# Kernel tuning notes

Hardware: AMD Instinct MI355X
Metric: run time of the kernel (lower is better)

## Reference

```python
import jax, jax.numpy as jnp
import numpy as np

NU = 0.01 / np.pi  # viscosity buffer from the torch module


def _mlp(x, W_in, b_in, W_hid, b_hid, W_out, b_out):
    # x: [N, 2] -> u: [N, 1]; tanh MLP with stacked hidden layers scanned.
    h = jnp.tanh(x @ W_in + b_in)

    def step(h, wb):
        W, b = wb
        return jnp.tanh(h @ W + b), None

    h, _ = jax.lax.scan(step, h, (W_hid, b_hid))
    return h @ W_out + b_out


def setup_inputs() -> dict:
    key = jax.random.key(0)
    ks = jax.random.split(key, 10)
    N_f, N0, Nb, H, L = 131072, 4096, 2048, 128, 7
    s_in = 1.0 / np.sqrt(2.0)
    s_h = 1.0 / np.sqrt(H)
    return {
        "x_f": jax.random.normal(ks[0], (N_f, 2), jnp.float32),
        "x0_cat": jax.random.normal(ks[1], (N0, 2), jnp.float32),
        "xb_left_cat": jax.random.normal(ks[2], (Nb, 2), jnp.float32),
        "xb_right_cat": jax.random.normal(ks[3], (Nb, 2), jnp.float32),
        "W_in": jax.random.normal(ks[4], (2, H), jnp.float32) * s_in,
        "b_in": jax.random.normal(ks[5], (H,), jnp.float32) * 0.01,
        "W_hid": jax.random.normal(ks[6], (L, H, H), jnp.float32) * s_h,
        "b_hid": jax.random.normal(ks[7], (L, H), jnp.float32) * 0.01,
        "W_out": jax.random.normal(ks[8], (H, 1), jnp.float32) * s_h,
        "b_out": jax.random.normal(ks[9], (1,), jnp.float32) * 0.01,
    }


def reference(x_f, x0_cat, xb_left_cat, xb_right_cat,
              W_in, b_in, W_hid, b_hid, W_out, b_out):
    u = lambda x: _mlp(x, W_in, b_in, W_hid, b_hid, W_out, b_out)

    u_0_pred = u(x0_cat)
    u_b_left_pred = u(xb_left_cat)
    u_b_right_pred = u(xb_right_cat)

    u_f_pred = u(x_f)  # [N_f, 1]

    # Each row of u depends only on the matching row of x, so grad of the sum
    # yields per-example gradients (equivalent to torch.autograd.grad with
    # grad_outputs=ones).
    usum = lambda x: u(x).sum()
    g = jax.grad(usum)(x_f)            # [N_f, 2]
    u_x = g[:, 0:1]
    u_t = g[:, 1:2]

    # Second derivative: grad of sum(u_x) w.r.t. x, take the x-component.
    uxx_full = jax.grad(lambda x: jax.grad(usum)(x)[:, 0].sum())(x_f)
    u_xx = uxx_full[:, 0:1]

    pde_residual = u_t + u_f_pred * u_x - NU * u_xx
    return jnp.concatenate((u_0_pred, u_b_left_pred, u_b_right_pred,
                            pde_residual), axis=0)
```

## Files before the change

### kernel.cpp

```cpp
#include <hip/hip_runtime.h>
#include <math.h>

#define NU_F 0.0031830988618379067f

typedef _Float16 f16x8 __attribute__((ext_vector_type(8)));
typedef float    f32x4 __attribute__((ext_vector_type(4)));

__device__ __forceinline__ float fast_tanh(float z) {
    float e = __builtin_amdgcn_exp2f(2.885390082f * z);
    float r = __builtin_amdgcn_rcpf(e + 1.0f);
    return fmaf(-2.0f, r, 1.0f);
}

__device__ __forceinline__ unsigned pkf16(float a, float b) {
    auto v = __builtin_amdgcn_cvt_pkrtz(a, b);
    return __builtin_bit_cast(unsigned, v);
}

__global__ void prep_wfrag(const float* __restrict__ Whid, _Float16* __restrict__ wcf)
{
    const int t    = blockIdx.x * 256 + threadIdx.x;
    const int lane = t & 63;
    const int fid  = t >> 6;
    const int ks = fid & 3;
    const int nt = (fid >> 2) & 7;
    const int l  = fid >> 5;
    const int q  = lane >> 4;
    const int nn = lane & 15;
    const int c  = ((nt >> 2) << 6) + nn * 4 + (nt & 3);
    const int k0 = ks * 32 + q * 8;
    const float* src = Whid + l * 16384 + k0 * 128 + c;
    f16x8 v;
    #pragma unroll
    for (int jj = 0; jj < 8; ++jj)
        v[jj] = (_Float16)src[jj * 128];
    *(f16x8*)(wcf + (size_t)t * 8) = v;
}

#define HR 68
#define MFMA(A, B, C) __builtin_amdgcn_mfma_f32_16x16x32_f16((A), (B), (C), 0, 0, 0)

__global__ __launch_bounds__(128, 3)
void pinn_fused(const float* __restrict__ xf,
                const float* __restrict__ x0,  const float* __restrict__ xbl,
                const float* __restrict__ xbr,
                const float* __restrict__ Win,  const float* __restrict__ bin,
                const float* __restrict__ bhid,
                const float* __restrict__ Wout, const float* __restrict__ bout,
                const _Float16* __restrict__ wcf,
                float* __restrict__ out)
{
    __shared__ unsigned Hh[64 * HR];
    __shared__ float xpt[128];
    __shared__ float pbuf[128];
    __shared__ float dots[64];

    const int tid  = threadIdx.x;
    const int lane = tid & 63;
    const int wv   = tid >> 6;
    const int lm   = lane & 15;
    const int lq   = lane >> 4;
    const int blk  = blockIdx.x;
    const bool isv = (blk >= 8192);

    if (!isv) {
        if (tid < 32) xpt[tid] = xf[blk * 32 + tid];
    } else {
        const int vb = blk - 8192;
        const float* src = (vb < 64) ? (x0 + vb * 128)
                         : (vb < 96) ? (xbl + (vb - 64) * 128)
                                     : (xbr + (vb - 96) * 128);
        xpt[tid] = src[tid];
    }
    __syncthreads();

    const int cp = tid & 63;
    {
        const float2 w01 = *(const float2*)&Win[cp * 2];
        const float2 w11 = *(const float2*)&Win[128 + cp * 2];
        const float2 bb  = *(const float2*)&bin[cp * 2];
        if (!isv) {
            const int p0 = (tid >> 6) * 8;
            #pragma unroll
            for (int i = 0; i < 8; ++i) {
                const int p = p0 + i;
                const float x = xpt[2 * p], tt = xpt[2 * p + 1];
                const float za = fmaf(x, w01.x, fmaf(tt, w11.x, bb.x));
                const float zb = fmaf(x, w01.y, fmaf(tt, w11.y, bb.y));
                const float ya = fast_tanh(za), yb = fast_tanh(zb);
                const float da = 1.f - ya * ya, db = 1.f - yb * yb;
                Hh[(0 * 16 + p) * HR + cp] = pkf16(ya, yb);
                Hh[(1 * 16 + p) * HR + cp] = pkf16(da * w01.x, db * w01.y);
                Hh[(2 * 16 + p) * HR + cp] = pkf16(da * w11.x, db * w11.y);
                Hh[(3 * 16 + p) * HR + cp] =
                    pkf16(-2.f * ya * da * w01.x * w01.x,
                          -2.f * yb * db * w01.y * w01.y);
            }
        } else {
            const int p0 = (tid >> 6) * 32;
            #pragma unroll
            for (int i = 0; i < 32; ++i) {
                const int p = p0 + i;
                const float x = xpt[2 * p], tt = xpt[2 * p + 1];
                const float za = fmaf(x, w01.x, fmaf(tt, w11.x, bb.x));
                const float zb = fmaf(x, w01.y, fmaf(tt, w11.y, bb.y));
                Hh[p * HR + cp] = pkf16(fast_tanh(za), fast_tanh(zb));
            }
        }
    }
    __syncthreads();

    const _Float16* pb0 = wcf + (wv * 4 + 0) * 2048 + lane * 8;
    const _Float16* pb1 = wcf + (wv * 4 + 1) * 2048 + lane * 8;
    const _Float16* pb2 = wcf + (wv * 4 + 2) * 2048 + lane * 8;
    const _Float16* pb3 = wcf + (wv * 4 + 3) * 2048 + lane * 8;
    const int wc = wv * 32 + lm * 2;

    if (!isv) {
        for (int l = 0; l < 7; ++l) {
            f32x4 acc[4][4];
            #pragma unroll
            for (int s = 0; s < 4; ++s)
                #pragma unroll
                for (int j = 0; j < 4; ++j) acc[s][j] = (f32x4){0.f, 0.f, 0.f, 0.f};

            #pragma unroll
            for (int ks = 0; ks < 4; ++ks) {
                const int ro = ks * 16 + lq * 4;
                const f16x8 ah0 = *(const f16x8*)&Hh[(0 * 16 + lm) * HR + ro];
                const f16x8 ah1 = *(const f16x8*)&Hh[(1 * 16 + lm) * HR + ro];
                const f16x8 ah2 = *(const f16x8*)&Hh[(2 * 16 + lm) * HR + ro];
                const f16x8 ah3 = *(const f16x8*)&Hh[(3 * 16 + lm) * HR + ro];
                const f16x8 b0 = *(const f16x8*)(pb0 + ks * 512);
                const f16x8 b1 = *(const f16x8*)(pb1 + ks * 512);
                const f16x8 b2 = *(const f16x8*)(pb2 + ks * 512);
                const f16x8 b3 = *(const f16x8*)(pb3 + ks * 512);
                acc[0][0] = MFMA(ah0, b0, acc[0][0]);
                acc[1][0] = MFMA(ah1, b0, acc[1][0]);
                acc[2][0] = MFMA(ah2, b0, acc[2][0]);
                acc[3][0] = MFMA(ah3, b0, acc[3][0]);
                acc[0][1] = MFMA(ah0, b1, acc[0][1]);
                acc[1][1] = MFMA(ah1, b1, acc[1][1]);
                acc[2][1] = MFMA(ah2, b1, acc[2][1]);
                acc[3][1] = MFMA(ah3, b1, acc[3][1]);
                acc[0][2] = MFMA(ah0, b2, acc[0][2]);
                acc[1][2] = MFMA(ah1, b2, acc[1][2]);
                acc[2][2] = MFMA(ah2, b2, acc[2][2]);
                acc[3][2] = MFMA(ah3, b2, acc[3][2]);
                acc[0][3] = MFMA(ah0, b3, acc[0][3]);
                acc[1][3] = MFMA(ah1, b3, acc[1][3]);
                acc[2][3] = MFMA(ah2, b3, acc[2][3]);
                acc[3][3] = MFMA(ah3, b3, acc[3][3]);
            }
            __syncthreads();

            float bb[4];
            *(float4*)bb = *(const float4*)&bhid[l * 128 + wv * 64 + lm * 4];
            #pragma unroll
            for (int r = 0; r < 4; ++r) {
                const int p = lq * 4 + r;
                float h[4][4];
                #pragma unroll
                for (int j = 0; j < 4; ++j) {
                    const float zv  = acc[0][j][r] + bb[j];
                    const float zx  = acc[1][j][r];
                    const float zt  = acc[2][j][r];
                    const float zxx = acc[3][j][r];
                    const float y = fast_tanh(zv);
                    const float d = fmaf(-y, y, 1.f);
                    const float m = d * zx;
                    h[j][0] = y;
                    h[j][1] = m;
                    h[j][2] = d * zt;
                    h[j][3] = fmaf(d, zxx, -2.f * (y * m) * zx);
                }
                #pragma unroll
                for (int s = 0; s < 4; ++s) {
                    uint2 w;
                    w.x = pkf16(h[0][s], h[1][s]);
                    w.y = pkf16(h[2][s], h[3][s]);
                    *(uint2*)&Hh[(s * 16 + p) * HR + wc] = w;
                }
            }
            pb0 += 16384; pb1 += 16384; pb2 += 16384; pb3 += 16384;
            __syncthreads();
        }
    } else {
        for (int l = 0; l < 7; ++l) {
            f32x4 acc[4][4];
            #pragma unroll
            for (int mt = 0; mt < 4; ++mt)
                #pragma unroll
                for (int j = 0; j < 4; ++j) acc[mt][j] = (f32x4){0.f, 0.f, 0.f, 0.f};

            #pragma unroll
            for (int ks = 0; ks < 4; ++ks) {
                const int ro = ks * 16 + lq * 4;
                f16x8 ah[4];
                #pragma unroll
                for (int mt = 0; mt < 4; ++mt)
                    ah[mt] = *(const f16x8*)&Hh[(mt * 16 + lm) * HR + ro];
                const f16x8 b0 = *(const f16x8*)(pb0 + ks * 512);
                const f16x8 b1 = *(const f16x8*)(pb1 + ks * 512);
                const f16x8 b2 = *(const f16x8*)(pb2 + ks * 512);
                const f16x8 b3 = *(const f16x8*)(pb3 + ks * 512);
                #pragma unroll
                for (int mt = 0; mt < 4; ++mt) {
                    acc[mt][0] = MFMA(ah[mt], b0, acc[mt][0]);
                    acc[mt][1] = MFMA(ah[mt], b1, acc[mt][1]);
                    acc[mt][2] = MFMA(ah[mt], b2, acc[mt][2]);
                    acc[mt][3] = MFMA(ah[mt], b3, acc[mt][3]);
                }
            }
            __syncthreads();

            float bb[4];
            *(float4*)bb = *(const float4*)&bhid[l * 128 + wv * 64 + lm * 4];
            #pragma unroll
            for (int mt = 0; mt < 4; ++mt) {
                #pragma unroll
                for (int r = 0; r < 4; ++r) {
                    const int p = mt * 16 + lq * 4 + r;
                    float y[4];
                    #pragma unroll
                    for (int j = 0; j < 4; ++j)
                        y[j] = fast_tanh(acc[mt][j][r] + bb[j]);
                    uint2 w;
                    w.x = pkf16(y[0], y[1]);
                    w.y = pkf16(y[2], y[3]);
                    *(uint2*)&Hh[p * HR + wc] = w;
                }
            }
            pb0 += 16384; pb1 += 16384; pb2 += 16384; pb3 += 16384;
            __syncthreads();
        }
    }

    {
        const int st = tid & 63;
        const int ch = tid >> 6;
        const int cb = ch * 32;
        float part = 0.f;
        #pragma unroll
        for (int c8 = 0; c8 < 8; ++c8) {
            const f16x8 hv = *(const f16x8*)&Hh[st * HR + cb + c8 * 4];
            const float4 w1 = *(const float4*)&Wout[ch * 64 + c8 * 8];
            const float4 w2 = *(const float4*)&Wout[ch * 64 + c8 * 8 + 4];
            part = fmaf((float)hv[0], w1.x, part);
            part = fmaf((float)hv[1], w1.y, part);
            part = fmaf((float)hv[2], w1.z, part);
            part = fmaf((float)hv[3], w1.w, part);
            part = fmaf((float)hv[4], w2.x, part);
            part = fmaf((float)hv[5], w2.y, part);
            part = fmaf((float)hv[6], w2.z, part);
            part = fmaf((float)hv[7], w2.w, part);
        }
        pbuf[ch * 64 + st] = part;
    }
    __syncthreads();
    if (tid < 64) dots[tid] = pbuf[tid] + pbuf[64 + tid];
    __syncthreads();
    if (!isv) {
        if (tid < 16) {
            const float u = dots[tid] + bout[0];
            out[8192 + blk * 16 + tid] =
                dots[32 + tid] + u * dots[16 + tid] - NU_F * dots[48 + tid];
        }
    } else {
        if (tid < 64) out[(blk - 8192) * 64 + tid] = dots[tid] + bout[0];
    }
}

extern "C" void kernel_launch(void* const* d_in, const int* in_sizes, int n_in,
                              void* d_out, int out_size, void* d_ws, size_t ws_size,
                              hipStream_t stream) {
    (void)in_sizes; (void)n_in; (void)ws_size; (void)out_size;
    const float* xf   = (const float*)d_in[0];
    const float* x0   = (const float*)d_in[1];
    const float* xbl  = (const float*)d_in[2];
    const float* xbr  = (const float*)d_in[3];
    const float* Win  = (const float*)d_in[4];
    const float* bin  = (const float*)d_in[5];
    const float* Whid = (const float*)d_in[6];
    const float* bhid = (const float*)d_in[7];
    const float* Wout = (const float*)d_in[8];
    const float* bout = (const float*)d_in[9];
    float* out = (float*)d_out;

    _Float16* wcf = (_Float16*)d_ws;

    hipLaunchKernelGGL(prep_wfrag, dim3(14336 / 256), dim3(256), 0, stream,
                       Whid, wcf);
    hipLaunchKernelGGL(pinn_fused, dim3(8192 + 128), dim3(128), 0, stream,
                       xf, x0, xbl, xbr, Win, bin, bhid, Wout, bout, wcf, out);
}
```

Before: 214.9 us.

## Split hidden-layer columns across four waves and prefold tanh scale into weights

Each block now runs 4 waves (256 threads) instead of 2, and each wave owns 32 output columns instead of 64, so per-wave accumulators and MFMA count per layer halve. The weight-fragment prep is remapped so each wave reads 2 B fragments. The 2/ln2 tanh scale is folded into input weights, biases and an FMA on the accumulator, which saves a multiply per tanh. In exchange, the A-fragment loads from LDS are duplicated across more waves and the output reduction now needs 4 partial sums.

```diff
diff --git a/kernel.cpp b/kernel.cpp
--- a/kernel.cpp
+++ b/kernel.cpp
@@ -2,12 +2,13 @@
 #include <math.h>
 
 #define NU_F 0.0031830988618379067f
+#define KTANH 2.885390082f
 
 typedef _Float16 f16x8 __attribute__((ext_vector_type(8)));
 typedef float    f32x4 __attribute__((ext_vector_type(4)));
 
-__device__ __forceinline__ float fast_tanh(float z) {
-    float e = __builtin_amdgcn_exp2f(2.885390082f * z);
+__device__ __forceinline__ float tanh_pre(float zs) {
+    float e = __builtin_amdgcn_exp2f(zs);
     float r = __builtin_amdgcn_rcpf(e + 1.0f);
     return fmaf(-2.0f, r, 1.0f);
 }
@@ -27,7 +28,7 @@
     const int l  = fid >> 5;
     const int q  = lane >> 4;
     const int nn = lane & 15;
-    const int c  = ((nt >> 2) << 6) + nn * 4 + (nt & 3);
+    const int c  = ((nt >> 1) << 5) + nn * 2 + (nt & 1);
     const int k0 = ks * 32 + q * 8;
     const float* src = Whid + l * 16384 + k0 * 128 + c;
     f16x8 v;
@@ -40,7 +41,7 @@
 #define HR 68
 #define MFMA(A, B, C) __builtin_amdgcn_mfma_f32_16x16x32_f16((A), (B), (C), 0, 0, 0)
 
-__global__ __launch_bounds__(128, 3)
+__global__ __launch_bounds__(256, 4)
 void pinn_fused(const float* __restrict__ xf,
                 const float* __restrict__ x0,  const float* __restrict__ xbl,
                 const float* __restrict__ xbr,
@@ -52,7 +53,7 @@
 {
     __shared__ unsigned Hh[64 * HR];
     __shared__ float xpt[128];
-    __shared__ float pbuf[128];
+    __shared__ float pbuf[256];
     __shared__ float dots[64];
 
     const int tid  = threadIdx.x;
@@ -66,11 +67,13 @@
     if (!isv) {
         if (tid < 32) xpt[tid] = xf[blk * 32 + tid];
     } else {
-        const int vb = blk - 8192;
-        const float* src = (vb < 64) ? (x0 + vb * 128)
-                         : (vb < 96) ? (xbl + (vb - 64) * 128)
-                                     : (xbr + (vb - 96) * 128);
-        xpt[tid] = src[tid];
+        if (tid < 128) {
+            const int vb = blk - 8192;
+            const float* src = (vb < 64) ? (x0 + vb * 128)
+                             : (vb < 96) ? (xbl + (vb - 64) * 128)
+                                         : (xbr + (vb - 96) * 128);
+            xpt[tid] = src[tid];
+        }
     }
     __syncthreads();
 
@@ -79,15 +82,17 @@
         const float2 w01 = *(const float2*)&Win[cp * 2];
         const float2 w11 = *(const float2*)&Win[128 + cp * 2];
         const float2 bb  = *(const float2*)&bin[cp * 2];
+        const float w01sx = w01.x * KTANH, w01sy = w01.y * KTANH;
+        const float w11sx = w11.x * KTANH, w11sy = w11.y * KTANH;
+        const float bbsx  = bb.x  * KTANH, bbsy  = bb.y  * KTANH;
         if (!isv) {
-            const int p0 = (tid >> 6) * 8;
-            #pragma unroll
-            for (int i = 0; i < 8; ++i) {
+            const int p0 = wv * 4;
+            #pragma unroll
+            for (int i = 0; i < 4; ++i) {
                 const int p = p0 + i;
                 const float x = xpt[2 * p], tt = xpt[2 * p + 1];
-                const float za = fmaf(x, w01.x, fmaf(tt, w11.x, bb.x));
-                const float zb = fmaf(x, w01.y, fmaf(tt, w11.y, bb.y));
-                const float ya = fast_tanh(za), yb = fast_tanh(zb);
+                const float ya = tanh_pre(fmaf(x, w01sx, fmaf(tt, w11sx, bbsx)));
+                const float yb = tanh_pre(fmaf(x, w01sy, fmaf(tt, w11sy, bbsy)));
                 const float da = 1.f - ya * ya, db = 1.f - yb * yb;
                 Hh[(0 * 16 + p) * HR + cp] = pkf16(ya, yb);
                 Hh[(1 * 16 + p) * HR + cp] = pkf16(da * w01.x, db * w01.y);
@@ -97,32 +102,36 @@
                           -2.f * yb * db * w01.y * w01.y);
             }
         } else {
-            const int p0 = (tid >> 6) * 32;
-            #pragma unroll
-            for (int i = 0; i < 32; ++i) {
+            const int p0 = wv * 16;
+            #pragma unroll
+            for (int i = 0; i < 16; ++i) {
                 const int p = p0 + i;
                 const float x = xpt[2 * p], tt = xpt[2 * p + 1];
-                const float za = fmaf(x, w01.x, fmaf(tt, w11.x, bb.x));
-                const float zb = fmaf(x, w01.y, fmaf(tt, w11.y, bb.y));
-                Hh[p * HR + cp] = pkf16(fast_tanh(za), fast_tanh(zb));
-            }
-        }
-    }
-    __syncthreads();
-
-    const _Float16* pb0 = wcf + (wv * 4 + 0) * 2048 + lane * 8;
-    const _Float16* pb1 = wcf + (wv * 4 + 1) * 2048 + lane * 8;
-    const _Float16* pb2 = wcf + (wv * 4 + 2) * 2048 + lane * 8;
-    const _Float16* pb3 = wcf + (wv * 4 + 3) * 2048 + lane * 8;
-    const int wc = wv * 32 + lm * 2;
+                const float ya = tanh_pre(fmaf(x, w01sx, fmaf(tt, w11sx, bbsx)));
+                const float yb = tanh_pre(fmaf(x, w01sy, fmaf(tt, w11sy, bbsy)));
+                Hh[p * HR + cp] = pkf16(ya, yb);
+            }
+        }
+    }
+    __syncthreads();
+
+    const _Float16* pb0 = wcf + (wv * 2 + 0) * 2048 + lane * 8;
+    const _Float16* pb1 = wcf + (wv * 2 + 1) * 2048 + lane * 8;
+    const int wc = wv * 16 + lm;
 
     if (!isv) {
         for (int l = 0; l < 7; ++l) {
-            f32x4 acc[4][4];
+            float bbs[2];
+            {
+                const float2 bt = *(const float2*)&bhid[l * 128 + wv * 32 + lm * 2];
+                bbs[0] = bt.x * KTANH; bbs[1] = bt.y * KTANH;
+            }
+
+            f32x4 acc[4][2];
             #pragma unroll
             for (int s = 0; s < 4; ++s)
                 #pragma unroll
-                for (int j = 0; j < 4; ++j) acc[s][j] = (f32x4){0.f, 0.f, 0.f, 0.f};
+                for (int j = 0; j < 2; ++j) acc[s][j] = (f32x4){0.f, 0.f, 0.f, 0.f};
 
             #pragma unroll
             for (int ks = 0; ks < 4; ++ks) {
@@ -133,8 +142,6 @@
                 const f16x8 ah3 = *(const f16x8*)&Hh[(3 * 16 + lm) * HR + ro];
                 const f16x8 b0 = *(const f16x8*)(pb0 + ks * 512);
                 const f16x8 b1 = *(const f16x8*)(pb1 + ks * 512);
-                const f16x8 b2 = *(const f16x8*)(pb2 + ks * 512);
-                const f16x8 b3 = *(const f16x8*)(pb3 + ks * 512);
                 acc[0][0] = MFMA(ah0, b0, acc[0][0]);
                 acc[1][0] = MFMA(ah1, b0, acc[1][0]);
                 acc[2][0] = MFMA(ah2, b0, acc[2][0]);
@@ -143,30 +150,19 @@
                 acc[1][1] = MFMA(ah1, b1, acc[1][1]);
                 acc[2][1] = MFMA(ah2, b1, acc[2][1]);
                 acc[3][1] = MFMA(ah3, b1, acc[3][1]);
-                acc[0][2] = MFMA(ah0, b2, acc[0][2]);
-                acc[1][2] = MFMA(ah1, b2, acc[1][2]);
-                acc[2][2] = MFMA(ah2, b2, acc[2][2]);
-                acc[3][2] = MFMA(ah3, b2, acc[3][2]);
-                acc[0][3] = MFMA(ah0, b3, acc[0][3]);
-                acc[1][3] = MFMA(ah1, b3, acc[1][3]);
-                acc[2][3] = MFMA(ah2, b3, acc[2][3]);
-                acc[3][3] = MFMA(ah3, b3, acc[3][3]);
-            }
-            __syncthreads();
-
-            float bb[4];
-            *(float4*)bb = *(const float4*)&bhid[l * 128 + wv * 64 + lm * 4];
+            }
+            __syncthreads();
+
             #pragma unroll
             for (int r = 0; r < 4; ++r) {
                 const int p = lq * 4 + r;
-                float h[4][4];
-                #pragma unroll
-                for (int j = 0; j < 4; ++j) {
-                    const float zv  = acc[0][j][r] + bb[j];
+                float h[2][4];
+                #pragma unroll
+                for (int j = 0; j < 2; ++j) {
                     const float zx  = acc[1][j][r];
                     const float zt  = acc[2][j][r];
                     const float zxx = acc[3][j][r];
-                    const float y = fast_tanh(zv);
+                    const float y = tanh_pre(fmaf(acc[0][j][r], KTANH, bbs[j]));
                     const float d = fmaf(-y, y, 1.f);
                     const float m = d * zx;
                     h[j][0] = y;
@@ -175,23 +171,25 @@
                     h[j][3] = fmaf(d, zxx, -2.f * (y * m) * zx);
                 }
                 #pragma unroll
-                for (int s = 0; s < 4; ++s) {
-                    uint2 w;
-                    w.x = pkf16(h[0][s], h[1][s]);
-                    w.y = pkf16(h[2][s], h[3][s]);
-                    *(uint2*)&Hh[(s * 16 + p) * HR + wc] = w;
-                }
-            }
-            pb0 += 16384; pb1 += 16384; pb2 += 16384; pb3 += 16384;
+                for (int s = 0; s < 4; ++s)
+                    Hh[(s * 16 + p) * HR + wc] = pkf16(h[0][s], h[1][s]);
+            }
+            pb0 += 16384; pb1 += 16384;
             __syncthreads();
         }
     } else {
         for (int l = 0; l < 7; ++l) {
-            f32x4 acc[4][4];
+            float bbs[2];
+            {
+                const float2 bt = *(const float2*)&bhid[l * 128 + wv * 32 + lm * 2];
+                bbs[0] = bt.x * KTANH; bbs[1] = bt.y * KTANH;
+            }
+
+            f32x4 acc[4][2];
             #pragma unroll
             for (int mt = 0; mt < 4; ++mt)
                 #pragma unroll
-                for (int j = 0; j < 4; ++j) acc[mt][j] = (f32x4){0.f, 0.f, 0.f, 0.f};
+                for (int j = 0; j < 2; ++j) acc[mt][j] = (f32x4){0.f, 0.f, 0.f, 0.f};
 
             #pragma unroll
             for (int ks = 0; ks < 4; ++ks) {
@@ -202,50 +200,39 @@
                     ah[mt] = *(const f16x8*)&Hh[(mt * 16 + lm) * HR + ro];
                 const f16x8 b0 = *(const f16x8*)(pb0 + ks * 512);
                 const f16x8 b1 = *(const f16x8*)(pb1 + ks * 512);
-                const f16x8 b2 = *(const f16x8*)(pb2 + ks * 512);
-                const f16x8 b3 = *(const f16x8*)(pb3 + ks * 512);
                 #pragma unroll
                 for (int mt = 0; mt < 4; ++mt) {
                     acc[mt][0] = MFMA(ah[mt], b0, acc[mt][0]);
                     acc[mt][1] = MFMA(ah[mt], b1, acc[mt][1]);
-                    acc[mt][2] = MFMA(ah[mt], b2, acc[mt][2]);
-                    acc[mt][3] = MFMA(ah[mt], b3, acc[mt][3]);
                 }
             }
             __syncthreads();
 
-            float bb[4];
-            *(float4*)bb = *(const float4*)&bhid[l * 128 + wv * 64 + lm * 4];
             #pragma unroll
             for (int mt = 0; mt < 4; ++mt) {
                 #pragma unroll
                 for (int r = 0; r < 4; ++r) {
                     const int p = mt * 16 + lq * 4 + r;
-                    float y[4];
-                    #pragma unroll
-                    for (int j = 0; j < 4; ++j)
-                        y[j] = fast_tanh(acc[mt][j][r] + bb[j]);
-                    uint2 w;
-                    w.x = pkf16(y[0], y[1]);
-                    w.y = pkf16(y[2], y[3]);
-                    *(uint2*)&Hh[p * HR + wc] = w;
+                    const float y0 = tanh_pre(fmaf(acc[mt][0][r], KTANH, bbs[0]));
+                    const float y1 = tanh_pre(fmaf(acc[mt][1][r], KTANH, bbs[1]));
+                    Hh[p * HR + wc] = pkf16(y0, y1);
                 }
             }
-            pb0 += 16384; pb1 += 16384; pb2 += 16384; pb3 += 16384;
+            pb0 += 16384; pb1 += 16384;
             __syncthreads();
         }
     }
 
     {
-        const int st = tid & 63;
-        const int ch = tid >> 6;
-        const int cb = ch * 32;
+        const int st = lane;
+        const int ch = wv;
+        const int cb = ch * 16;
         float part = 0.f;
         #pragma unroll
-        for (int c8 = 0; c8 < 8; ++c8) {
+        for (int c8 = 0; c8 < 4; ++c8) {
             const f16x8 hv = *(const f16x8*)&Hh[st * HR + cb + c8 * 4];
-            const float4 w1 = *(const float4*)&Wout[ch * 64 + c8 * 8];
-            const float4 w2 = *(const float4*)&Wout[ch * 64 + c8 * 8 + 4];
+            const float4 w1 = *(const float4*)&Wout[ch * 32 + c8 * 8];
+            const float4 w2 = *(const float4*)&Wout[ch * 32 + c8 * 8 + 4];
             part = fmaf((float)hv[0], w1.x, part);
             part = fmaf((float)hv[1], w1.y, part);
             part = fmaf((float)hv[2], w1.z, part);
@@ -258,7 +245,8 @@
         pbuf[ch * 64 + st] = part;
     }
     __syncthreads();
-    if (tid < 64) dots[tid] = pbuf[tid] + pbuf[64 + tid];
+    if (tid < 64)
+        dots[tid] = (pbuf[tid] + pbuf[64 + tid]) + (pbuf[128 + tid] + pbuf[192 + tid]);
     __syncthreads();
     if (!isv) {
         if (tid < 16) {
@@ -291,6 +279,6 @@
 
     hipLaunchKernelGGL(prep_wfrag, dim3(14336 / 256), dim3(256), 0, stream,
                        Whid, wcf);
-    hipLaunchKernelGGL(pinn_fused, dim3(8192 + 128), dim3(128), 0, stream,
+    hipLaunchKernelGGL(pinn_fused, dim3(8192 + 128), dim3(256), 0, stream,
                        xf, x0, xbl, xbr, Win, bin, bhid, Wout, bout, wcf, out);
 }
```

After: 219.4 us. 1.02x slower.
